# Kernel tuning notes

Measured on AMD Instinct MI355X. Metric: run time of the kernel, lower is better.

Reference implementation:

```python
import jax, jax.numpy as jnp
import numpy as np

VOCAB = 50257
DIM = 768
B, S = 8, 2048

def setup_inputs() -> dict:
    key = jax.random.key(0)
    k1, k2 = jax.random.split(key)
    x = jax.random.randint(k1, (B, S), 0, VOCAB, dtype=jnp.int64 if jax.config.jax_enable_x64 else jnp.int32)
    weight = jax.random.normal(k2, (VOCAB, DIM), dtype=jnp.float32)
    return {"x": x, "weight": weight}

def reference(x, weight):
    # Embedding lookup: gather rows of weight by token id -> [B, S, DIM]
    return weight[x]
```

## Files before the change

### kernel.cpp

```cpp
#include <hip/hip_runtime.h>
#include <hip/hip_bf16.h>


typedef float f32x4 __attribute__((ext_vector_type(4)));

__global__ void __launch_bounds__(256)
embed_gather_kernel(const int* __restrict__ x,
                    const f32x4* __restrict__ w,
                    f32x4* __restrict__ out,
                    int n_tokens) {
    const int wave = threadIdx.x >> 6;
    const int lane = threadIdx.x & 63;
    const int tokens_per_iter = gridDim.x * 4;

    for (int token = blockIdx.x * 4 + wave; token < n_tokens; token += tokens_per_iter) {
        const int row = x[token];
        const f32x4* __restrict__ src = w + (size_t)row * 192;
        f32x4* __restrict__ dst = out + (size_t)token * 192;

        f32x4 a = src[lane];
        f32x4 b = src[lane + 64];
        f32x4 c = src[lane + 128];

        __builtin_nontemporal_store(a, &dst[lane]);
        __builtin_nontemporal_store(b, &dst[lane + 64]);
        __builtin_nontemporal_store(c, &dst[lane + 128]);
    }
}

extern "C" void kernel_launch(void* const* d_in, const int* in_sizes, int n_in,
                              void* d_out, int out_size, void* d_ws, size_t ws_size,
                              hipStream_t stream) {
    const int* x = (const int*)d_in[0];
    const float* weight = (const float*)d_in[1];
    float* out = (float*)d_out;

    const int n_tokens = in_sizes[0];

    int blocks = (n_tokens + 3) / 4;
    embed_gather_kernel<<<blocks, 256, 0, stream>>>(
        x, (const f32x4*)weight, (f32x4*)out, n_tokens);
}
```

Measured before the change: 20.59 us.

## Process four tokens per wave with software-pipelined row prefetch

Each wave now handles four consecutive tokens instead of one. It loads the next token's embedding row before storing the current one, so loads and stores overlap inside the wave. The grid shrinks by four times, which may lower the number of waves in flight for hiding memory latency. It also adds register pressure for the double-buffered vectors.

```diff
diff --git a/kernel.cpp b/kernel.cpp
--- a/kernel.cpp
+++ b/kernel.cpp
@@ -3,6 +3,8 @@
 
 
 typedef float f32x4 __attribute__((ext_vector_type(4)));
+
+constexpr int TPW = 4;
 
 __global__ void __launch_bounds__(256)
 embed_gather_kernel(const int* __restrict__ x,
@@ -11,20 +13,31 @@
                     int n_tokens) {
     const int wave = threadIdx.x >> 6;
     const int lane = threadIdx.x & 63;
-    const int tokens_per_iter = gridDim.x * 4;
+    const int wid  = blockIdx.x * 4 + wave;
+    int t = wid * TPW;
+    if (t >= n_tokens) return;
 
-    for (int token = blockIdx.x * 4 + wave; token < n_tokens; token += tokens_per_iter) {
-        const int row = x[token];
-        const f32x4* __restrict__ src = w + (size_t)row * 192;
-        f32x4* __restrict__ dst = out + (size_t)token * 192;
+    int row = x[t];
+    const f32x4* __restrict__ s = w + (size_t)row * 192;
+    f32x4 a = s[lane], b = s[lane + 64], c = s[lane + 128];
 
-        f32x4 a = src[lane];
-        f32x4 b = src[lane + 64];
-        f32x4 c = src[lane + 128];
-
+    #pragma unroll
+    for (int i = 0; i < TPW; ++i) {
+        f32x4 a2, b2, c2;
+        if (i + 1 < TPW && t + 1 < n_tokens) {
+            const int row2 = x[t + 1];
+            const f32x4* __restrict__ s2 = w + (size_t)row2 * 192;
+            a2 = s2[lane];
+            b2 = s2[lane + 64];
+            c2 = s2[lane + 128];
+        }
+        f32x4* __restrict__ dst = out + (size_t)t * 192;
         __builtin_nontemporal_store(a, &dst[lane]);
         __builtin_nontemporal_store(b, &dst[lane + 64]);
         __builtin_nontemporal_store(c, &dst[lane + 128]);
+        a = a2; b = b2; c = c2;
+        ++t;
+        if (t >= n_tokens) return;
     }
 }
 
@@ -36,8 +49,8 @@
     float* out = (float*)d_out;
 
     const int n_tokens = in_sizes[0];
-
-    int blocks = (n_tokens + 3) / 4;
+    const int n_waves  = (n_tokens + TPW - 1) / TPW;
+    const int blocks   = (n_waves + 3) / 4;
     embed_gather_kernel<<<blocks, 256, 0, stream>>>(
         x, (const f32x4*)weight, (f32x4*)out, n_tokens);
 }
```

Measured after the change: 20.60 us. Within noise of the previous version (+0.1%).
